# Kernel tuning notes

Measured on AMD Instinct MI355X. Metric: run time of the kernel, lower is better.

The kernel has to match this reference:

```python
import jax, jax.numpy as jnp
import numpy as np

B, C, H, N = 4, 128, 4, 2048
D = C // H  # head_dim = 32
BN_EPS = 1e-5


def _conv1(w, b, x):
    # 1x1 Conv1d: [O,C] x [B,C,N] -> [B,O,N]
    return jnp.einsum('oc,bcn->bon', w, x) + b[None, :, None]


def setup_inputs() -> dict:
    key = jax.random.key(0)
    ks = jax.random.split(key, 20)
    p = lambda k, shape: jax.random.normal(k, shape, dtype=jnp.float32) * 0.05
    return {
        'x1': jax.random.normal(ks[0], (B, C, N), dtype=jnp.float32),
        'x2': jax.random.normal(ks[1], (B, C, N), dtype=jnp.float32),
        'kv_mask': jnp.ones((B, N), dtype=bool),
        'wq': p(ks[2], (C, C)), 'bq': p(ks[3], (C,)),
        'wk': p(ks[4], (C, C)), 'bk': p(ks[5], (C,)),
        'wv': p(ks[6], (C, C)), 'bv': p(ks[7], (C,)),
        'wm': p(ks[8], (C, C)), 'bm': p(ks[9], (C,)),
        'wc1': p(ks[10], (2 * C, 2 * C)), 'bc1': p(ks[11], (2 * C,)),
        'bn_gamma': jnp.ones((2 * C,), dtype=jnp.float32),
        'bn_beta': jnp.zeros((2 * C,), dtype=jnp.float32),
        'bn_mean': p(ks[12], (2 * C,)),
        'bn_var': jax.random.uniform(ks[13], (2 * C,), dtype=jnp.float32, minval=0.5, maxval=1.5),
        'wc2': p(ks[14], (C, 2 * C)), 'bc2': p(ks[15], (C,)),
    }


def reference(x1, x2, kv_mask, wq, bq, wk, bk, wv, bv, wm, bm,
              wc1, bc1, bn_gamma, bn_beta, bn_mean, bn_var, wc2, bc2):
    b, _, n = x1.shape
    q = _conv1(wq, bq, x1).reshape(b, H, D, n)   # bhdn
    k = _conv1(wk, bk, x2).reshape(b, H, D, -1)  # bhdm
    v = _conv1(wv, bv, x2).reshape(b, H, D, -1)  # bhdm
    qk = jnp.einsum('bhdn,bhdm->bhnm', q, k)
    # masked_fill on raw QK before scaling, matching torch code
    qk = jnp.where(kv_mask[:, None, None, :], qk, jnp.float32(-1e6))
    score = jax.nn.softmax(qk * (1.0 / D ** 0.5), axis=-1)
    add_value = jnp.einsum('bhnm,bhdm->bhdn', score, v).reshape(b, C, n)
    add_value = _conv1(wm, bm, add_value)
    cat = jnp.concatenate([x1, add_value], axis=1)  # [B, 2C, N]
    h = _conv1(wc1, bc1, cat)
    # BatchNorm1d in inference mode (running stats)
    h = (h - bn_mean[None, :, None]) * jax.lax.rsqrt(bn_var[None, :, None] + BN_EPS)
    h = h * bn_gamma[None, :, None] + bn_beta[None, :, None]
    h = jax.nn.relu(h)
    h = _conv1(wc2, bc2, h)
    return x1 + h
```

## Files before the change

### kernel.cpp

```cpp
#include <hip/hip_runtime.h>

typedef __attribute__((ext_vector_type(4))) float v4f;
typedef __attribute__((ext_vector_type(8))) _Float16 half8;
typedef __attribute__((ext_vector_type(4))) _Float16 half4;
typedef __attribute__((ext_vector_type(2))) _Float16 half2t;

constexpr float C2 = 0.17677669529663687f * 1.44269504088896341f;

__device__ __forceinline__ half4 pk4(float a, float b, float c, float d) {
  half2t lo = __builtin_bit_cast(half2t, __builtin_amdgcn_cvt_pkrtz(a, b));
  half2t hi = __builtin_bit_cast(half2t, __builtin_amdgcn_cvt_pkrtz(c, d));
  return __builtin_shufflevector(lo, hi, 0, 1, 2, 3);
}
__device__ __forceinline__ half8 pk8f4(const float4 a, const float4 b) {
  const half4 lo = pk4(a.x, a.y, a.z, a.w);
  const half4 hi = pk4(b.x, b.y, b.z, b.w);
  return __builtin_shufflevector(lo, hi, 0, 1, 2, 3, 4, 5, 6, 7);
}

__global__ __launch_bounds__(512) void qkv(
    const float* __restrict__ x1, const float* __restrict__ x2,
    const float* __restrict__ wq, const float* __restrict__ bq,
    const float* __restrict__ wk, const float* __restrict__ bk,
    const float* __restrict__ wv, const float* __restrict__ bv,
    const float* __restrict__ wm, const float* __restrict__ wc1,
    const float* __restrict__ wc2, const unsigned char* __restrict__ mask,
    _Float16* __restrict__ Qpk, _Float16* __restrict__ Kpk,
    _Float16* __restrict__ Vpk, _Float16* __restrict__ wts,
    float* __restrict__ maskf) {
  const int b = blockIdx.y;
  const int bx = blockIdx.x;
  const int tid = threadIdx.x, w = tid >> 6, lane = tid & 63;
  const int l = lane & 15, q = lane >> 4;
  const int n = bx * 16 + l;

  if (b == 0 && bx < 72) {
    const int e = (bx * 512 + tid) * 4;
    const float* src;
    int base;
    if (e < 16384) { src = wm; base = 0; }
    else if (e < 81920) { src = wc1; base = 16384; }
    else { src = wc2; base = 81920; }
    const float4 t = *(const float4*)(src + (e - base));
    *(half4*)(wts + e) = pk4(t.x, t.y, t.z, t.w);
  } else if (b == 1 && bx < 4) {
    const int e = (bx * 512 + tid) * 4;
    const unsigned mv = *(const unsigned*)(mask + e);
    float4 o;
    o.x = (mv & 0x000000ffu) ? 0.f : -1.0e6f * C2;
    o.y = (mv & 0x0000ff00u) ? 0.f : -1.0e6f * C2;
    o.z = (mv & 0x00ff0000u) ? 0.f : -1.0e6f * C2;
    o.w = (mv & 0xff000000u) ? 0.f : -1.0e6f * C2;
    *(float4*)(maskf + e) = o;
  }

  half8 x1f[4], x2f[4];
#pragma unroll
  for (int kt = 0; kt < 4; ++kt) {
    float4 a, c;
    const size_t rb = (size_t)(b * 128 + kt * 32 + q * 8) * 2048 + n;
    a.x = x1[rb]; a.y = x1[rb + 2048]; a.z = x1[rb + 4096]; a.w = x1[rb + 6144];
    c.x = x1[rb + 8192]; c.y = x1[rb + 10240]; c.z = x1[rb + 12288]; c.w = x1[rb + 14336];
    x1f[kt] = pk8f4(a, c);
    a.x = x2[rb]; a.y = x2[rb + 2048]; a.z = x2[rb + 4096]; a.w = x2[rb + 6144];
    c.x = x2[rb + 8192]; c.y = x2[rb + 10240]; c.z = x2[rb + 12288]; c.w = x2[rb + 14336];
    x2f[kt] = pk8f4(a, c);
  }

#pragma unroll
  for (int i = 0; i < 3; ++i) {
    const int t = w * 3 + i;
    if (t < 8) {
      const int mt = t;
      v4f acc = *(const v4f*)(bq + mt * 16 + q * 4);
#pragma unroll
      for (int kt = 0; kt < 4; ++kt) {
        const float4 wa = *(const float4*)(wq + (mt * 16 + l) * 128 + kt * 32 + q * 8);
        const float4 wb = *(const float4*)(wq + (mt * 16 + l) * 128 + kt * 32 + q * 8 + 4);
        acc = __builtin_amdgcn_mfma_f32_16x16x32_f16(pk8f4(wa, wb), x1f[kt], acc, 0, 0, 0);
      }
      *(half4*)(Qpk + ((size_t)(b * 8 + mt) * 2048 + n) * 16 + q * 4) =
          pk4(acc[0] * C2, acc[1] * C2, acc[2] * C2, acc[3] * C2);
    } else if (t < 16) {
      const int mt = t - 8;
      v4f acc = *(const v4f*)(bk + mt * 16 + q * 4);
#pragma unroll
      for (int kt = 0; kt < 4; ++kt) {
        const float4 wa = *(const float4*)(wk + (mt * 16 + l) * 128 + kt * 32 + q * 8);
        const float4 wb = *(const float4*)(wk + (mt * 16 + l) * 128 + kt * 32 + q * 8 + 4);
        acc = __builtin_amdgcn_mfma_f32_16x16x32_f16(pk8f4(wa, wb), x2f[kt], acc, 0, 0, 0);
      }
      *(half4*)(Kpk + ((size_t)(b * 8 + mt) * 2048 + n) * 16 + q * 4) =
          pk4(acc[0], acc[1], acc[2], acc[3]);
    } else {
      const int ot = t - 16;
      const float bvv = bv[ot * 16 + l];
      v4f acc = {bvv, bvv, bvv, bvv};
#pragma unroll
      for (int kt = 0; kt < 4; ++kt) {
        const float4 wa = *(const float4*)(wv + (ot * 16 + l) * 128 + kt * 32 + q * 8);
        const float4 wb = *(const float4*)(wv + (ot * 16 + l) * 128 + kt * 32 + q * 8 + 4);
        acc = __builtin_amdgcn_mfma_f32_16x16x32_f16(x2f[kt], pk8f4(wa, wb), acc, 0, 0, 0);
      }
      *(half4*)(Vpk + (((size_t)(b * 4 + (ot >> 1)) * 128 + bx) * 32 +
                       (ot & 1) * 16 + l) * 16 + q * 4) =
          pk4(acc[0], acc[1], acc[2], acc[3]);
    }
  }
}

__global__ __launch_bounds__(256) void attn(
    const _Float16* __restrict__ Qpk, const _Float16* __restrict__ Kpk,
    const _Float16* __restrict__ Vpk, const float* __restrict__ maskf,
    _Float16* __restrict__ Opk, float* __restrict__ lsump) {
  const int bh = blockIdx.y, b = bh >> 2, h = bh & 3;
  const int part = blockIdx.z;
  const int tid = threadIdx.x, w = tid >> 6, lane = tid & 63;
  const int l = lane & 15, q = lane >> 4;
  const int nb = blockIdx.x * 128 + w * 32;

  const size_t qrow = (size_t)(b * 8 + h * 2 + (q >> 1)) * 2048;
  const half8 qf0 = *(const half8*)(Qpk + (qrow + nb + l) * 16 + (q & 1) * 8);
  const half8 qf1 = *(const half8*)(Qpk + (qrow + nb + 16 + l) * 16 + (q & 1) * 8);
  const _Float16* __restrict__ Kb = Kpk + qrow * 16 + (q & 1) * 8;
  const _Float16* __restrict__ Vb =
      Vpk + ((size_t)(b * 4 + h) * 128) * 512 + (size_t)l * 16 + q * 4;
  const float* __restrict__ mf = maskf + b * 2048;

  v4f oacc[2][2] = {{{0.f, 0.f, 0.f, 0.f}, {0.f, 0.f, 0.f, 0.f}},
                    {{0.f, 0.f, 0.f, 0.f}, {0.f, 0.f, 0.f, 0.f}}};
  float ls0 = 0.f, ls1 = 0.f;

  const int mbeg = part * 512;
  for (int m0 = mbeg; m0 < mbeg + 512; m0 += 64) {
    half4 pB[2][4];
#pragma unroll
    for (int mt = 0; mt < 4; ++mt) {
      const half8 kf = *(const half8*)(Kb + (size_t)(m0 + mt * 16 + l) * 16);
      const v4f biasv = *(const v4f*)(mf + m0 + mt * 16 + q * 4);
      const v4f s0 = __builtin_amdgcn_mfma_f32_16x16x32_f16(kf, qf0, biasv, 0, 0, 0);
      const v4f s1 = __builtin_amdgcn_mfma_f32_16x16x32_f16(kf, qf1, biasv, 0, 0, 0);
      const float a0 = exp2f(s0[0]), a1 = exp2f(s0[1]), a2 = exp2f(s0[2]),
                  a3 = exp2f(s0[3]);
      const float c0 = exp2f(s1[0]), c1 = exp2f(s1[1]), c2 = exp2f(s1[2]),
                  c3 = exp2f(s1[3]);
      ls0 += (a0 + a1) + (a2 + a3);
      ls1 += (c0 + c1) + (c2 + c3);
      pB[0][mt] = pk4(a0, a1, a2, a3);
      pB[1][mt] = pk4(c0, c1, c2, c3);
    }
#pragma unroll
    for (int mt = 0; mt < 4; ++mt) {
      const size_t vbase = (size_t)((m0 >> 4) + mt) * 512;
      const half4 vf0 = *(const half4*)(Vb + vbase);
      const half4 vf1 = *(const half4*)(Vb + vbase + 256);
      oacc[0][0] = __builtin_amdgcn_mfma_f32_16x16x16f16(vf0, pB[0][mt], oacc[0][0], 0, 0, 0);
      oacc[0][1] = __builtin_amdgcn_mfma_f32_16x16x16f16(vf1, pB[0][mt], oacc[0][1], 0, 0, 0);
      oacc[1][0] = __builtin_amdgcn_mfma_f32_16x16x16f16(vf0, pB[1][mt], oacc[1][0], 0, 0, 0);
      oacc[1][1] = __builtin_amdgcn_mfma_f32_16x16x16f16(vf1, pB[1][mt], oacc[1][1], 0, 0, 0);
    }
  }
  ls0 += __shfl_xor(ls0, 16);
  ls0 += __shfl_xor(ls0, 32);
  ls1 += __shfl_xor(ls1, 16);
  ls1 += __shfl_xor(ls1, 32);
  if (q == 0) {
    lsump[part * 32768 + bh * 2048 + nb + l] = ls0;
    lsump[part * 32768 + bh * 2048 + nb + 16 + l] = ls1;
  }
#pragma unroll
  for (int qt = 0; qt < 2; ++qt)
#pragma unroll
    for (int df = 0; df < 2; ++df)
      *(half4*)(Opk + (size_t)part * 1048576 +
                ((size_t)(b * 8 + h * 2 + df) * 2048 + nb + qt * 16 + l) * 16 +
                q * 4) = pk4(oacc[qt][df][0], oacc[qt][df][1], oacc[qt][df][2],
                             oacc[qt][df][3]);
}

__global__ __launch_bounds__(512) void post(
    const float* __restrict__ x1, const _Float16* __restrict__ Opk,
    const float* __restrict__ lsump, const _Float16* __restrict__ wts,
    const float* __restrict__ bm, const float* __restrict__ bc1,
    const float* __restrict__ gamma, const float* __restrict__ beta,
    const float* __restrict__ mean, const float* __restrict__ var,
    const float* __restrict__ bc2, float* __restrict__ out) {
  const int b = blockIdx.y;
  const int n0 = blockIdx.x * 16;
  const int tid = threadIdx.x, w = tid >> 6, lane = tid & 63;
  const int l = lane & 15, q = lane >> 4;
  const int n = n0 + l;
  const _Float16* wm_h = wts;
  const _Float16* wc1_h = wts + 16384;
  const _Float16* wc2_h = wts + 81920;

  __shared__ _Float16 exA[8 * 256];
  __shared__ _Float16 exB[16 * 256];

  float rlh[4];
#pragma unroll
  for (int hh = 0; hh < 4; ++hh) {
    const size_t idx = (size_t)(b * 4 + hh) * 2048 + n;
    rlh[hh] = 1.0f / (lsump[idx] + lsump[32768 + idx] + lsump[65536 + idx] +
                      lsump[98304 + idx]);
  }
  half4 of[8];
#pragma unroll
  for (int kt = 0; kt < 8; ++kt) {
    const size_t oa = ((size_t)(b * 8 + kt) * 2048 + n) * 16 + q * 4;
    const half4 a = *(const half4*)(Opk + oa);
    const half4 c = *(const half4*)(Opk + 1048576 + oa);
    const half4 d = *(const half4*)(Opk + 2097152 + oa);
    const half4 e = *(const half4*)(Opk + 3145728 + oa);
    const _Float16 rh = (_Float16)rlh[kt >> 1];
    const half4 rl4 = {rh, rh, rh, rh};
    of[kt] = ((a + c) + (d + e)) * rl4;
  }
  half4 catf[16];
  float xr[4];
#pragma unroll
  for (int kt = 0; kt < 8; ++kt) {
    const float v0 = x1[(size_t)(b * 128 + kt * 16 + q * 4 + 0) * 2048 + n];
    const float v1 = x1[(size_t)(b * 128 + kt * 16 + q * 4 + 1) * 2048 + n];
    const float v2 = x1[(size_t)(b * 128 + kt * 16 + q * 4 + 2) * 2048 + n];
    const float v3 = x1[(size_t)(b * 128 + kt * 16 + q * 4 + 3) * 2048 + n];
    if (kt == w) { xr[0] = v0; xr[1] = v1; xr[2] = v2; xr[3] = v3; }
    catf[kt] = pk4(v0, v1, v2, v3);
  }
  {
    v4f acc = *(const v4f*)(bm + w * 16 + q * 4);
#pragma unroll
    for (int kt = 0; kt < 8; ++kt) {
      const half4 wf = *(const half4*)(wm_h + (w * 16 + l) * 128 + kt * 16 + q * 4);
      acc = __builtin_amdgcn_mfma_f32_16x16x16f16(wf, of[kt], acc, 0, 0, 0);
    }
    *(half4*)&exA[w * 256 + l * 16 + q * 4] = pk4(acc[0], acc[1], acc[2], acc[3]);
  }
  __syncthreads();
#pragma unroll
  for (int f = 0; f < 8; ++f)
    catf[8 + f] = *(const half4*)&exA[f * 256 + l * 16 + q * 4];
#pragma unroll
  for (int i = 0; i < 2; ++i) {
    const int mt = w * 2 + i;
    v4f acc = *(const v4f*)(bc1 + mt * 16 + q * 4);
#pragma unroll
    for (int kt = 0; kt < 16; ++kt) {
      const half4 wf = *(const half4*)(wc1_h + (mt * 16 + l) * 256 + kt * 16 + q * 4);
      acc = __builtin_amdgcn_mfma_f32_16x16x16f16(wf, catf[kt], acc, 0, 0, 0);
    }
    const v4f g = *(const v4f*)(gamma + mt * 16 + q * 4);
    const v4f bt = *(const v4f*)(beta + mt * 16 + q * 4);
    const v4f mn = *(const v4f*)(mean + mt * 16 + q * 4);
    const v4f vr = *(const v4f*)(var + mt * 16 + q * 4);
    float hh[4];
#pragma unroll
    for (int r = 0; r < 4; ++r) {
      const float a1 = g[r] * rsqrtf(vr[r] + 1e-5f);
      const float b1 = bt[r] - mn[r] * a1;
      hh[r] = fmaxf(acc[r] * a1 + b1, 0.f);
    }
    *(half4*)&exB[mt * 256 + l * 16 + q * 4] = pk4(hh[0], hh[1], hh[2], hh[3]);
  }
  __syncthreads();
  {
    v4f acc = *(const v4f*)(bc2 + w * 16 + q * 4);
#pragma unroll
    for (int kt = 0; kt < 16; ++kt) {
      const half4 hfv = *(const half4*)&exB[kt * 256 + l * 16 + q * 4];
      const half4 wf = *(const half4*)(wc2_h + (w * 16 + l) * 256 + kt * 16 + q * 4);
      acc = __builtin_amdgcn_mfma_f32_16x16x16f16(wf, hfv, acc, 0, 0, 0);
    }
#pragma unroll
    for (int r = 0; r < 4; ++r)
      out[(size_t)(b * 128 + w * 16 + q * 4 + r) * 2048 + n] = acc[r] + xr[r];
  }
}

extern "C" void kernel_launch(void* const* d_in, const int* in_sizes, int n_in,
                              void* d_out, int out_size, void* d_ws,
                              size_t ws_size, hipStream_t stream) {
  const float* x1 = (const float*)d_in[0];
  const float* x2 = (const float*)d_in[1];
  const unsigned char* kv_mask = (const unsigned char*)d_in[2];
  const float* wq = (const float*)d_in[3];
  const float* bq = (const float*)d_in[4];
  const float* wk = (const float*)d_in[5];
  const float* bk = (const float*)d_in[6];
  const float* wv = (const float*)d_in[7];
  const float* bv = (const float*)d_in[8];
  const float* wm = (const float*)d_in[9];
  const float* bm = (const float*)d_in[10];
  const float* wc1 = (const float*)d_in[11];
  const float* bc1 = (const float*)d_in[12];
  const float* bn_gamma = (const float*)d_in[13];
  const float* bn_beta = (const float*)d_in[14];
  const float* bn_mean = (const float*)d_in[15];
  const float* bn_var = (const float*)d_in[16];
  const float* wc2 = (const float*)d_in[17];
  const float* bc2 = (const float*)d_in[18];
  float* out = (float*)d_out;

  char* p = (char*)d_ws;
  _Float16* Qpk = (_Float16*)p;
  _Float16* Kpk = (_Float16*)(p + (size_t)2 * 1024 * 1024);
  _Float16* Vpk = (_Float16*)(p + (size_t)4 * 1024 * 1024);
  _Float16* Opk = (_Float16*)(p + (size_t)6 * 1024 * 1024);
  _Float16* wts = (_Float16*)(p + (size_t)14 * 1024 * 1024);
  float* lsump = (float*)(p + (size_t)14 * 1024 * 1024 + 512 * 1024);
  float* maskf = lsump + 4 * 32768;

  qkv<<<dim3(128, 4), 512, 0, stream>>>(x1, x2, wq, bq, wk, bk, wv, bv, wm,
                                        wc1, wc2, kv_mask, Qpk, Kpk, Vpk, wts,
                                        maskf);
  attn<<<dim3(16, 16, 4), 256, 0, stream>>>(Qpk, Kpk, Vpk, maskf, Opk, lsump);
  post<<<dim3(128, 4), 512, 0, stream>>>(x1, Opk, lsump, wts, bm, bc1,
                                         bn_gamma, bn_beta, bn_mean, bn_var,
                                         bc2, out);
}
```

Before: 170.4 us.

## Stage K/V tiles through double-buffered LDS and transpose x inputs via shared memory

In the attention kernel, the 4 waves of a block now cooperatively load each 64-key tile of K and V into padded, double-buffered shared memory, prefetching the next tile into registers during compute. Previously every wave read the same K/V fragments from global memory on its own. In the qkv kernel, x1/x2 are read with coalesced float4 loads, converted to fp16 and transposed through LDS, replacing strided scalar global loads. This adds __syncthreads barriers and LDS traffic, and may reduce occupancy.

```diff
diff --git a/kernel.cpp b/kernel.cpp
--- a/kernel.cpp
+++ b/kernel.cpp
@@ -32,7 +32,11 @@
   const int bx = blockIdx.x;
   const int tid = threadIdx.x, w = tid >> 6, lane = tid & 63;
   const int l = lane & 15, q = lane >> 4;
-  const int n = bx * 16 + l;
+  const int n0 = bx * 16;
+  const int n = n0 + l;
+
+  __shared__ _Float16 x1s[16 * 136];
+  __shared__ _Float16 x2s[16 * 136];
 
   if (b == 0 && bx < 72) {
     const int e = (bx * 512 + tid) * 4;
@@ -54,17 +58,26 @@
     *(float4*)(maskf + e) = o;
   }
 
+  {
+    const int ch = tid >> 2, seg = tid & 3;
+    const float4 a = *(const float4*)(x1 + (size_t)(b * 128 + ch) * 2048 + n0 + seg * 4);
+    const float4 c = *(const float4*)(x2 + (size_t)(b * 128 + ch) * 2048 + n0 + seg * 4);
+    x1s[(seg * 4 + 0) * 136 + ch] = (_Float16)a.x;
+    x1s[(seg * 4 + 1) * 136 + ch] = (_Float16)a.y;
+    x1s[(seg * 4 + 2) * 136 + ch] = (_Float16)a.z;
+    x1s[(seg * 4 + 3) * 136 + ch] = (_Float16)a.w;
+    x2s[(seg * 4 + 0) * 136 + ch] = (_Float16)c.x;
+    x2s[(seg * 4 + 1) * 136 + ch] = (_Float16)c.y;
+    x2s[(seg * 4 + 2) * 136 + ch] = (_Float16)c.z;
+    x2s[(seg * 4 + 3) * 136 + ch] = (_Float16)c.w;
+  }
+  __syncthreads();
+
   half8 x1f[4], x2f[4];
 #pragma unroll
   for (int kt = 0; kt < 4; ++kt) {
-    float4 a, c;
-    const size_t rb = (size_t)(b * 128 + kt * 32 + q * 8) * 2048 + n;
-    a.x = x1[rb]; a.y = x1[rb + 2048]; a.z = x1[rb + 4096]; a.w = x1[rb + 6144];
-    c.x = x1[rb + 8192]; c.y = x1[rb + 10240]; c.z = x1[rb + 12288]; c.w = x1[rb + 14336];
-    x1f[kt] = pk8f4(a, c);
-    a.x = x2[rb]; a.y = x2[rb + 2048]; a.z = x2[rb + 4096]; a.w = x2[rb + 6144];
-    c.x = x2[rb + 8192]; c.y = x2[rb + 10240]; c.z = x2[rb + 12288]; c.w = x2[rb + 14336];
-    x2f[kt] = pk8f4(a, c);
+    x1f[kt] = *(const half8*)&x1s[l * 136 + kt * 32 + q * 8];
+    x2f[kt] = *(const half8*)&x2s[l * 136 + kt * 32 + q * 8];
   }
 
 #pragma unroll
@@ -119,24 +132,42 @@
   const int l = lane & 15, q = lane >> 4;
   const int nb = blockIdx.x * 128 + w * 32;
 
+  __shared__ _Float16 ldsK[2][3088];
+  __shared__ _Float16 ldsV[2][3072];
+
   const size_t qrow = (size_t)(b * 8 + h * 2 + (q >> 1)) * 2048;
   const half8 qf0 = *(const half8*)(Qpk + (qrow + nb + l) * 16 + (q & 1) * 8);
   const half8 qf1 = *(const half8*)(Qpk + (qrow + nb + 16 + l) * 16 + (q & 1) * 8);
-  const _Float16* __restrict__ Kb = Kpk + qrow * 16 + (q & 1) * 8;
-  const _Float16* __restrict__ Vb =
-      Vpk + ((size_t)(b * 4 + h) * 128) * 512 + (size_t)l * 16 + q * 4;
+  const _Float16* __restrict__ Kg = Kpk + (size_t)(b * 8 + h * 2) * 2048 * 16;
+  const _Float16* __restrict__ Vg = Vpk + (size_t)((b * 4 + h) * 128) * 512;
   const float* __restrict__ mf = maskf + b * 2048;
+
+  const int kct = tid >> 7, kk = (tid >> 1) & 63, khf = tid & 1;
+  const int vt = tid >> 6, vd = (tid >> 1) & 31;
 
   v4f oacc[2][2] = {{{0.f, 0.f, 0.f, 0.f}, {0.f, 0.f, 0.f, 0.f}},
                     {{0.f, 0.f, 0.f, 0.f}, {0.f, 0.f, 0.f, 0.f}}};
   float ls0 = 0.f, ls1 = 0.f;
-
   const int mbeg = part * 512;
-  for (int m0 = mbeg; m0 < mbeg + 512; m0 += 64) {
+
+  half8 kr = *(const half8*)(Kg + ((size_t)kct * 2048 + mbeg + kk) * 16 + khf * 8);
+  half8 vr = *(const half8*)(Vg + (size_t)((mbeg >> 4) + vt) * 512 + vd * 16 + khf * 8);
+  *(half8*)&ldsK[0][kct * 1544 + kk * 24 + khf * 8] = kr;
+  *(half8*)&ldsV[0][vt * 768 + vd * 24 + khf * 8] = vr;
+  __syncthreads();
+
+  for (int i = 0; i < 8; ++i) {
+    const int m0 = mbeg + i * 64;
+    const int cur = i & 1;
+    if (i < 7) {
+      kr = *(const half8*)(Kg + ((size_t)kct * 2048 + m0 + 64 + kk) * 16 + khf * 8);
+      vr = *(const half8*)(Vg + (size_t)(((m0 + 64) >> 4) + vt) * 512 + vd * 16 + khf * 8);
+    }
     half4 pB[2][4];
 #pragma unroll
     for (int mt = 0; mt < 4; ++mt) {
-      const half8 kf = *(const half8*)(Kb + (size_t)(m0 + mt * 16 + l) * 16);
+      const half8 kf =
+          *(const half8*)&ldsK[cur][(q >> 1) * 1544 + (mt * 16 + l) * 24 + (q & 1) * 8];
       const v4f biasv = *(const v4f*)(mf + m0 + mt * 16 + q * 4);
       const v4f s0 = __builtin_amdgcn_mfma_f32_16x16x32_f16(kf, qf0, biasv, 0, 0, 0);
       const v4f s1 = __builtin_amdgcn_mfma_f32_16x16x32_f16(kf, qf1, biasv, 0, 0, 0);
@@ -151,13 +182,17 @@
     }
 #pragma unroll
     for (int mt = 0; mt < 4; ++mt) {
-      const size_t vbase = (size_t)((m0 >> 4) + mt) * 512;
-      const half4 vf0 = *(const half4*)(Vb + vbase);
-      const half4 vf1 = *(const half4*)(Vb + vbase + 256);
+      const half4 vf0 = *(const half4*)&ldsV[cur][mt * 768 + l * 24 + q * 4];
+      const half4 vf1 = *(const half4*)&ldsV[cur][mt * 768 + (16 + l) * 24 + q * 4];
       oacc[0][0] = __builtin_amdgcn_mfma_f32_16x16x16f16(vf0, pB[0][mt], oacc[0][0], 0, 0, 0);
       oacc[0][1] = __builtin_amdgcn_mfma_f32_16x16x16f16(vf1, pB[0][mt], oacc[0][1], 0, 0, 0);
       oacc[1][0] = __builtin_amdgcn_mfma_f32_16x16x16f16(vf0, pB[1][mt], oacc[1][0], 0, 0, 0);
       oacc[1][1] = __builtin_amdgcn_mfma_f32_16x16x16f16(vf1, pB[1][mt], oacc[1][1], 0, 0, 0);
+    }
+    if (i < 7) {
+      *(half8*)&ldsK[cur ^ 1][kct * 1544 + kk * 24 + khf * 8] = kr;
+      *(half8*)&ldsV[cur ^ 1][vt * 768 + vd * 24 + khf * 8] = vr;
+      __syncthreads();
     }
   }
   ls0 += __shfl_xor(ls0, 16);
```

After: 168.0 us. No clear change (-1.4%).
